# Optimization experiments

Hardware: AMD Instinct MI355X
Metric: run time of the kernel (lower is better)

Reference implementation:

```python
import jax, jax.numpy as jnp
import numpy as np

N = 4096
E = 262144
IN_DIM = 256
EDGE_DIM = 16
NUM_ATOM_FEATURES = 16
LATENT_DIM = 128
NUM_BOND_TYPES = 5


def setup_inputs() -> dict:
    key = jax.random.key(0)
    ks = jax.random.split(key, 12)
    inp = {
        's': jax.random.normal(ks[0], (N, IN_DIM), dtype=jnp.float32),
        'e': jax.random.normal(ks[1], (E, EDGE_DIM), dtype=jnp.float32),
        'batch': jnp.zeros((N,), dtype=jnp.int64),
        'edge_index_global': jax.random.randint(ks[2], (2, E), 0, N, dtype=jnp.int64),
        # learned parameters (torch nn.Linear layout: W is [out, in])
        'W_shared': jax.random.normal(ks[3], (IN_DIM, IN_DIM), dtype=jnp.float32) * 0.02,
        'b_shared': jnp.zeros((IN_DIM,), dtype=jnp.float32),
        'W_bond': jax.random.normal(ks[4], (IN_DIM, EDGE_DIM), dtype=jnp.float32) * 0.02,
        'b_bond': jnp.zeros((IN_DIM,), dtype=jnp.float32),
        'W_bonds': jax.random.normal(ks[5], (NUM_BOND_TYPES, IN_DIM), dtype=jnp.float32) * 0.02,
        'b_bonds': jnp.zeros((NUM_BOND_TYPES,), dtype=jnp.float32),
        'W_atoms': jax.random.normal(ks[6], (NUM_ATOM_FEATURES + LATENT_DIM, IN_DIM), dtype=jnp.float32) * 0.02,
        'b_atoms': jnp.zeros((NUM_ATOM_FEATURES + LATENT_DIM,), dtype=jnp.float32),
    }
    return inp


def reference(s, e, batch, edge_index_global,
              W_shared, b_shared, W_bond, b_bond,
              W_bonds, b_bonds, W_atoms, b_atoms):
    # shared_mapping: Linear + SiLU
    s = jax.nn.silu(s @ W_shared.T + b_shared)  # [n, in_dim]
    j = edge_index_global[0]
    i = edge_index_global[1]
    n = s.shape[0]

    # atoms_lin then split into atom-type logits and latent prediction
    atoms_out = s @ W_atoms.T + b_atoms  # [n, num_atom_features + latent_dim]
    atoms_pred = atoms_out[:, :NUM_ATOM_FEATURES]
    latent_pred = atoms_out[:, NUM_ATOM_FEATURES:]

    # dense scatter -> symmetrize -> gather (faithful to the original O(n^2) path)
    e_dense = jnp.zeros((n, n, e.shape[-1]), dtype=e.dtype).at[j, i].set(e)
    e_dense = 0.5 * (e_dense + e_dense.transpose(1, 0, 2))
    e_sym = e_dense[j, i]  # [E, edge_dim]

    # fused gather + bond linear + SiLU + bonds linear
    f = jax.nn.silu(s[i] + s[j] + e_sym @ W_bond.T + b_bond)  # [E, in_dim]
    bonds_pred = f @ W_bonds.T + b_bonds  # [E, num_bond_types]

    return (latent_pred, atoms_pred, bonds_pred)
```

## Files before the change

### kernel.cpp

```cpp
#include <hip/hip_runtime.h>
#include <hip/hip_bf16.h>

#define N_NODES   4096
#define E_EDGES   262144
#define IN_DIM    256
#define EDGE_DIM  16
#define NAF       16
#define LATENT    128
#define NBT       5

#define LATENT_OFF 0
#define ATOMS_OFF  (N_NODES * LATENT)
#define BONDS_OFF  (ATOMS_OFF + N_NODES * NAF)

#define TBITS 20
#define TSIZE (1u << TBITS)
#define TMASK (TSIZE - 1u)

typedef float    f32x4  __attribute__((ext_vector_type(4)));
typedef float    f32x4v __attribute__((ext_vector_type(4)));
typedef short    bf16x8 __attribute__((ext_vector_type(8)));
typedef unsigned u32x2  __attribute__((ext_vector_type(2)));
typedef unsigned u32x4  __attribute__((ext_vector_type(4)));

__device__ __forceinline__ float silu_f(float x) {
    return x * __builtin_amdgcn_rcpf(1.0f + __expf(-x));
}

__device__ __forceinline__ unsigned pack_bf16x2(float lo, float hi) {
#if __has_builtin(__builtin_amdgcn_cvt_pk_bf16_f32)
    typedef __bf16 bf16x2_t __attribute__((ext_vector_type(2)));
    union { bf16x2_t v; unsigned u; } c;
    c.v = __builtin_amdgcn_cvt_pk_bf16_f32(lo, hi);
    return c.u;
#else
    union { float f; unsigned u; } a, b;
    a.f = lo; b.f = hi;
    const unsigned ra = (a.u + 0x7FFFu + ((a.u >> 16) & 1u)) >> 16;
    const unsigned rb = (b.u + 0x7FFFu + ((b.u >> 16) & 1u)) >> 16;
    return ra | (rb << 16);
#endif
}

__device__ __forceinline__ float bf_lo(unsigned u) {
    union { unsigned x; float f; } c; c.x = u << 16; return c.f;
}
__device__ __forceinline__ float bf_hi(unsigned u) {
    union { unsigned x; float f; } c; c.x = u & 0xFFFF0000u; return c.f;
}

__device__ __forceinline__ void split_bf16(const float4 x0, const float4 x1,
                                           bf16x8* hi, bf16x8* lo) {
    union { bf16x8 v; unsigned u[4]; } H, L;
    H.u[0] = pack_bf16x2(x0.x, x0.y);
    H.u[1] = pack_bf16x2(x0.z, x0.w);
    H.u[2] = pack_bf16x2(x1.x, x1.y);
    H.u[3] = pack_bf16x2(x1.z, x1.w);
    L.u[0] = pack_bf16x2(x0.x - bf_lo(H.u[0]), x0.y - bf_hi(H.u[0]));
    L.u[1] = pack_bf16x2(x0.z - bf_lo(H.u[1]), x0.w - bf_hi(H.u[1]));
    L.u[2] = pack_bf16x2(x1.x - bf_lo(H.u[2]), x1.y - bf_hi(H.u[2]));
    L.u[3] = pack_bf16x2(x1.z - bf_lo(H.u[3]), x1.w - bf_hi(H.u[3]));
    *hi = H.v; *lo = L.v;
}

__device__ __forceinline__ void gld_lds16(const void* g, void* l) {
    __builtin_amdgcn_global_load_lds(
        (const __attribute__((address_space(1))) unsigned*)g,
        (__attribute__((address_space(3))) unsigned*)l, 16, 0, 0);
}

__device__ __forceinline__ unsigned hashh(unsigned key) {
    return (key * 2654435761u) >> (32 - TBITS);
}

__device__ __forceinline__ int resolve2(const unsigned long long* __restrict__ tab,
                                        unsigned key, unsigned long long s0,
                                        unsigned long long s1, unsigned h) {
    if ((unsigned)(s0 >> 18) == key + 1u) return (int)(s0 & 0x3FFFFu);
    if (s0 == 0ULL) return -1;
    if ((unsigned)(s1 >> 18) == key + 1u) return (int)(s1 & 0x3FFFFu);
    if (s1 == 0ULL) return -1;
    h = (h + 2u) & TMASK;
    while (true) {
        const unsigned long long cur = tab[h];
        if (cur == 0ULL) return -1;
        if ((unsigned)(cur >> 18) == key + 1u) return (int)(cur & 0x3FFFFu);
        h = (h + 1u) & TMASK;
    }
}

__global__ __launch_bounds__(256) void k_front(const float* __restrict__ s,
                                               const float* __restrict__ Wsh,
                                               const float* __restrict__ bsh,
                                               const int* __restrict__ eidx,
                                               const float* __restrict__ Wb,
                                               const float* __restrict__ bb,
                                               const float* __restrict__ Wbs,
                                               unsigned short* __restrict__ sact16,
                                               unsigned long long* __restrict__ tab,
                                               u32x4* __restrict__ A1pre,
                                               u32x4* __restrict__ A2pre) {
    const int blk = blockIdx.x;
    const int c   = threadIdx.x;

    if (blk >= 1024) {
        if (blk < 2048) {
            const int k = (blk - 1024) * 256 + c;
            const unsigned j = (unsigned)eidx[k];
            const unsigned i = (unsigned)eidx[E_EDGES + k];
            const unsigned key = (j << 12) | i;
            const unsigned long long mine =
                ((unsigned long long)(key + 1u) << 18) | (unsigned)k;
            unsigned h = hashh(key);
            while (true) {
                const unsigned long long old = atomicCAS(&tab[h], 0ULL, mine);
                if (old == 0ULL) return;
                if ((unsigned)(old >> 18) == key + 1u) {
                    atomicMax(&tab[h], mine);
                    return;
                }
                h = (h + 1u) & TMASK;
            }
        } else {
#pragma unroll
            for (int ee = 0; ee < 4; ++ee) {
                const int idx  = c + 256 * ee;
                const int g    = idx >> 6;
                const int lane = idx & 63;
                const int mm   = lane & 15;
                const int qq   = lane >> 4;

                const float4 w = *(const float4*)(Wb + (16 * g + mm) * EDGE_DIM + 4 * qq);
                u32x4 r1;
                r1.x = pack_bf16x2(w.x, w.y);
                r1.y = pack_bf16x2(w.z, w.w);
                r1.z = pack_bf16x2(bb[16 * g + mm], 0.0f);
                r1.w = 0u;
                A1pre[idx] = r1;

                u32x4 r2;
                if (mm < NBT) {
                    const float4 ws = *(const float4*)(Wbs + mm * IN_DIM + 16 * g + 4 * qq);
                    r2.x = pack_bf16x2(ws.x, ws.y);
                    r2.y = pack_bf16x2(ws.z, ws.w);
                } else {
                    r2.x = 0u; r2.y = 0u;
                }
                r2.z = 0u; r2.w = 0u;
                A2pre[idx] = r2;
            }
        }
        return;
    }

    const int lane = c & 63;
    const int wv   = c >> 6;
    const int wave = blk * 4 + wv;
    const int m    = lane & 15;
    const int q    = lane >> 4;
    const int row0 = (wave >> 4) * 16;
    const int col0 = (wave & 15) * 16;

    f32x4v acc;
    {
        const float bias = bsh[col0 + m];
        acc[0] = bias; acc[1] = bias; acc[2] = bias; acc[3] = bias;
    }

    const float* ap = s   + (size_t)(row0 + m) * IN_DIM + 8 * q;
    const float* bp = Wsh + (size_t)(col0 + m) * IN_DIM + 8 * q;

#pragma unroll
    for (int c8 = 0; c8 < 8; ++c8) {
        const float4 a0 = *(const float4*)(ap + 32 * c8);
        const float4 a1 = *(const float4*)(ap + 32 * c8 + 4);
        const float4 b0 = *(const float4*)(bp + 32 * c8);
        const float4 b1 = *(const float4*)(bp + 32 * c8 + 4);
        bf16x8 Ah, Al, Bh, Bl;
        split_bf16(a0, a1, &Ah, &Al);
        split_bf16(b0, b1, &Bh, &Bl);
        acc = __builtin_amdgcn_mfma_f32_16x16x32_bf16(Ah, Bh, acc, 0, 0, 0);
        acc = __builtin_amdgcn_mfma_f32_16x16x32_bf16(Al, Bh, acc, 0, 0, 0);
        acc = __builtin_amdgcn_mfma_f32_16x16x32_bf16(Ah, Bl, acc, 0, 0, 0);
    }

#pragma unroll
    for (int r = 0; r < 4; ++r) {
        const int row = row0 + 4 * q + r;
        const float v = silu_f(acc[r]);
        sact16[(size_t)row * IN_DIM + col0 + m] =
            (unsigned short)(pack_bf16x2(v, 0.0f) & 0xFFFFu);
    }
}

#define SB0()    __builtin_amdgcn_sched_barrier(0)
#define LGKM0()  do { __asm__ __volatile__("s_waitcnt lgkmcnt(0)" ::: "memory"); SB0(); } while (0)
#define VMW(n)   do { __asm__ __volatile__("s_waitcnt vmcnt(" #n ")" ::: "memory"); SB0(); } while (0)

__global__ __launch_bounds__(256, 6) void k_edges_mfma(const int* __restrict__ eidx,
                                                       const float* __restrict__ e,
                                                       const unsigned long long* __restrict__ tab,
                                                       const unsigned short* __restrict__ sact16,
                                                       const u32x4* __restrict__ A1pre,
                                                       const u32x4* __restrict__ A2pre,
                                                       const float* __restrict__ bbs,
                                                       const float* __restrict__ Wa,
                                                       const float* __restrict__ ba,
                                                       float* __restrict__ out) {
    __shared__ unsigned lds_all[4][1536];
    const int blk  = blockIdx.x;
    const int lane = threadIdx.x & 63;
    const int wv   = threadIdx.x >> 6;
    const int m    = lane & 15;
    const int q    = lane >> 4;

    if (blk >= 4096) {
        const int wave = (blk - 4096) * 4 + wv;
        const int rt = wave / 9;
        const int ct = wave - rt * 9;
        const int row0  = rt * 16;
        const int n_abs = ct * 16 + m;

        f32x4v acc;
        {
            const float bias = ba[n_abs];
            acc[0] = bias; acc[1] = bias; acc[2] = bias; acc[3] = bias;
        }

        const unsigned short* apu = sact16 + (size_t)(row0 + m) * IN_DIM + 8 * q;
        const float*          bp  = Wa + (size_t)n_abs * IN_DIM + 8 * q;

#pragma unroll
        for (int c8 = 0; c8 < 8; ++c8) {
            const bf16x8 A = *(const bf16x8*)(apu + 32 * c8);
            const float4 b0 = *(const float4*)(bp + 32 * c8);
            const float4 b1 = *(const float4*)(bp + 32 * c8 + 4);
            bf16x8 Bh, Bl;
            split_bf16(b0, b1, &Bh, &Bl);
            acc = __builtin_amdgcn_mfma_f32_16x16x32_bf16(A, Bh, acc, 0, 0, 0);
            acc = __builtin_amdgcn_mfma_f32_16x16x32_bf16(A, Bl, acc, 0, 0, 0);
        }
#pragma unroll
        for (int r = 0; r < 4; ++r) {
            const int row = row0 + 4 * q + r;
            if (n_abs < NAF)
                out[ATOMS_OFF + (size_t)row * NAF + n_abs] = acc[r];
            else
                out[LATENT_OFF + (size_t)row * LATENT + (n_abs - NAF)] = acc[r];
        }
        return;
    }

    const int k0 = __builtin_amdgcn_readfirstlane((blk * 4 + wv) * 16);
    unsigned* myl = lds_all[wv];
    const short one_q0 = (q == 0) ? (short)0x3F80 : (short)0;

    f32x4v acc_init;
#pragma unroll
    for (int r = 0; r < 4; ++r) {
        const int bond = 4 * q + r;
        acc_init[r] = (bond < NBT) ? bbs[bond] : 0.0f;
    }
    const u32x4* a1p = A1pre + lane;
    const u32x4* a2p = A2pre + lane;
    const int qh = q >> 1;
    const int qw = 2 * (q & 1);
    const int mw = m * 4;

    const unsigned j_m = (unsigned)eidx[k0 + m];
    const unsigned i_m = (unsigned)eidx[E_EDGES + k0 + m];

    const char* si_base = (const char*)(sact16 + (size_t)i_m * IN_DIM);
    const char* sj_base = (const char*)(sact16 + (size_t)j_m * IN_DIM);

    const unsigned keyF = (j_m << 12) | i_m, keyR = (i_m << 12) | j_m;
    const unsigned hF = hashh(keyF), hR = hashh(keyR);
    const unsigned long long sF0 = tab[hF];
    const unsigned long long sF1 = tab[(hF + 1u) & TMASK];
    const unsigned long long sR0 = tab[hR];
    const unsigned long long sR1 = tab[(hR + 1u) & TMASK];

    auto stage_e = [&](int p, int qb) {
        gld_lds16(si_base + p * 64 + q * 16, (char*)myl + qb);
        gld_lds16(sj_base + p * 64 + q * 16, (char*)myl + qb + 1024);
        SB0();
    };

    stage_e(0, 0);
    stage_e(1, 2048);
    stage_e(2, 4096);

    const int wf = resolve2(tab, keyF, sF0, sF1, hF);
    const int wr = resolve2(tab, keyR, sR0, sR1, hR);

    const float rsc = (wr >= 0) ? 0.5f : 0.0f;
    const int   wrc = (wr >= 0) ? wr : 0;
    const f32x4 ef = *(const f32x4*)(e + (size_t)wf  * EDGE_DIM + 4 * q);
    const f32x4 er = *(const f32x4*)(e + (size_t)wrc * EDGE_DIM + 4 * q);

    union { bf16x8 v; short s[8]; unsigned u[4]; } B1;
    {
        const f32x4 es = ef * 0.5f + er * rsc;
        B1.u[0] = pack_bf16x2(es[0], es[1]);
        B1.u[1] = pack_bf16x2(es[2], es[3]);
        B1.s[4] = one_q0; B1.s[5] = 0;
        B1.u[3] = 0u;
    }

    f32x4v acc0 = acc_init;
    f32x4v acc1 = {0.0f, 0.0f, 0.0f, 0.0f};

    auto qcompute2 = [&](int qb4, int gbase) {
#pragma unroll
        for (int gp = 0; gp < 2; ++gp) {
            const int g   = gbase + gp;
            const int off = (2 * gp + qh) * 64 + mw + qw;

            const u32x2 wi = *(const u32x2*)(myl + qb4 + off);
            const u32x2 wj = *(const u32x2*)(myl + qb4 + 256 + off);

            f32x4v C1;
            C1[0] = bf_lo(wi.x) + bf_lo(wj.x);
            C1[1] = bf_hi(wi.x) + bf_hi(wj.x);
            C1[2] = bf_lo(wi.y) + bf_lo(wj.y);
            C1[3] = bf_hi(wi.y) + bf_hi(wj.y);

            const u32x4 r1 = a1p[g * 64];
            const u32x4 r2 = a2p[g * 64];
            union { bf16x8 v; unsigned u[4]; } A1, A2;
            A1.u[0] = r1.x; A1.u[1] = r1.y; A1.u[2] = r1.z; A1.u[3] = 0u;
            A2.u[0] = r2.x; A2.u[1] = r2.y; A2.u[2] = 0u;   A2.u[3] = 0u;

            const f32x4v P = __builtin_amdgcn_mfma_f32_16x16x32_bf16(A1.v, B1.v, C1, 0, 0, 0);

            union { bf16x8 v; unsigned u[4]; } B2;
            B2.u[0] = pack_bf16x2(silu_f(P[0]), silu_f(P[1]));
            B2.u[1] = pack_bf16x2(silu_f(P[2]), silu_f(P[3]));
            B2.u[2] = 0u; B2.u[3] = 0u;

            if (gp & 1) acc1 = __builtin_amdgcn_mfma_f32_16x16x32_bf16(A2.v, B2.v, acc1, 0, 0, 0);
            else        acc0 = __builtin_amdgcn_mfma_f32_16x16x32_bf16(A2.v, B2.v, acc0, 0, 0, 0);
        }
    };

    VMW(0);
    qcompute2(0, 0);
    LGKM0(); stage_e(3, 0);

    VMW(2);
    qcompute2(512, 2);
    LGKM0(); stage_e(4, 2048);

    VMW(4);
    qcompute2(1024, 4);
    LGKM0(); stage_e(5, 4096);

    VMW(4);
    qcompute2(0, 6);
    LGKM0(); stage_e(6, 0);

    VMW(4);
    qcompute2(512, 8);
    LGKM0(); stage_e(7, 2048);

    VMW(4);
    qcompute2(1024, 10);

    VMW(2);
    qcompute2(0, 12);

    VMW(0);
    qcompute2(512, 14);

    const f32x4v accT = acc0 + acc1;
    float* op = out + BONDS_OFF + (size_t)(k0 + m) * NBT;
    if (q == 0) {
        op[0] = accT[0];
        op[1] = accT[1];
        op[2] = accT[2];
        op[3] = accT[3];
    } else if (q == 1) {
        op[4] = accT[0];
    }
}

extern "C" void kernel_launch(void* const* d_in, const int* in_sizes, int n_in,
                              void* d_out, int out_size, void* d_ws, size_t ws_size,
                              hipStream_t stream) {
    const float* s   = (const float*)d_in[0];
    const float* e   = (const float*)d_in[1];
    const int*   eix = (const int*)d_in[3];
    const float* Wsh = (const float*)d_in[4];
    const float* bsh = (const float*)d_in[5];
    const float* Wb  = (const float*)d_in[6];
    const float* bbo = (const float*)d_in[7];
    const float* Wbs = (const float*)d_in[8];
    const float* bbs = (const float*)d_in[9];
    const float* Wa  = (const float*)d_in[10];
    const float* ba  = (const float*)d_in[11];
    float* out = (float*)d_out;

    char* ws = (char*)d_ws;
    unsigned short*     sact16 = (unsigned short*)ws;
    u32x4*              A1pre  = (u32x4*)(ws + (2u << 20));
    u32x4*              A2pre  = (u32x4*)(ws + (2u << 20) + 16384);
    unsigned long long* tab    = (unsigned long long*)(ws + (3u << 20));

    (void)hipMemsetAsync(tab, 0x00, TSIZE * sizeof(unsigned long long), stream);

    k_front<<<2049, 256, 0, stream>>>(s, Wsh, bsh, eix, Wb, bbo, Wbs,
                                      sact16, tab, A1pre, A2pre);
    k_edges_mfma<<<4672, 256, 0, stream>>>(eix, e, tab, sact16,
                                           A1pre, A2pre, bbs, Wa, ba, out);
}
```

Measured before the change: 174.8 us.

## Stage W_shared in LDS and compute two column tiles per wave in front GEMM

The shared-mapping GEMM in k_front now gives each block a 64x32 output tile. The block converts its 32 rows of W_shared to bf16 hi/lo once into shared memory, and each wave reuses its split A fragment across two 16-column MFMA tiles. This removes the repeated global loads and bf16 splitting of W for every 16x16 tile, and the GEMM grid drops from 1024 to 512 blocks. It adds an LDS footprint, a block barrier, and fewer waves doing GEMM work. A minor indexing change to the A1pre/A2pre pointers in the edge kernel comes along with it.

```diff
diff --git a/kernel.cpp b/kernel.cpp
--- a/kernel.cpp
+++ b/kernel.cpp
@@ -100,12 +100,15 @@
                                                unsigned long long* __restrict__ tab,
                                                u32x4* __restrict__ A1pre,
                                                u32x4* __restrict__ A2pre) {
+    __shared__ short sWh[32][264];
+    __shared__ short sWl[32][264];
+
     const int blk = blockIdx.x;
     const int c   = threadIdx.x;
 
-    if (blk >= 1024) {
-        if (blk < 2048) {
-            const int k = (blk - 1024) * 256 + c;
+    if (blk >= 512) {
+        if (blk < 1536) {
+            const int k = (blk - 512) * 256 + c;
             const unsigned j = (unsigned)eidx[k];
             const unsigned i = (unsigned)eidx[E_EDGES + k];
             const unsigned key = (j << 12) | i;
@@ -153,43 +156,74 @@
         return;
     }
 
+    const int rg = blk >> 3;
+    const int cg = blk & 7;
+
+    {
+        const int r  = c >> 3;
+        const int cq = c & 7;
+        const float* wrow = Wsh + (size_t)(cg * 32 + r) * IN_DIM;
+#pragma unroll
+        for (int k = 0; k < 4; ++k) {
+            const int ch = cq + 8 * k;
+            const float4 b0 = *(const float4*)(wrow + ch * 8);
+            const float4 b1 = *(const float4*)(wrow + ch * 8 + 4);
+            bf16x8 Bh, Bl;
+            split_bf16(b0, b1, &Bh, &Bl);
+            *(bf16x8*)&sWh[r][ch * 8] = Bh;
+            *(bf16x8*)&sWl[r][ch * 8] = Bl;
+        }
+    }
+    __syncthreads();
+
     const int lane = c & 63;
     const int wv   = c >> 6;
-    const int wave = blk * 4 + wv;
     const int m    = lane & 15;
     const int q    = lane >> 4;
-    const int row0 = (wave >> 4) * 16;
-    const int col0 = (wave & 15) * 16;
-
-    f32x4v acc;
+    const int row0 = rg * 64 + wv * 16;
+
+    f32x4v acc0, acc1;
     {
-        const float bias = bsh[col0 + m];
-        acc[0] = bias; acc[1] = bias; acc[2] = bias; acc[3] = bias;
-    }
-
-    const float* ap = s   + (size_t)(row0 + m) * IN_DIM + 8 * q;
-    const float* bp = Wsh + (size_t)(col0 + m) * IN_DIM + 8 * q;
+        const float b0 = bsh[cg * 32 + m];
+        const float b1 = bsh[cg * 32 + 16 + m];
+        acc0[0] = b0; acc0[1] = b0; acc0[2] = b0; acc0[3] = b0;
+        acc1[0] = b1; acc1[1] = b1; acc1[2] = b1; acc1[3] = b1;
+    }
+
+    const float* ap = s + (size_t)(row0 + m) * IN_DIM + 8 * q;
 
 #pragma unroll
     for (int c8 = 0; c8 < 8; ++c8) {
         const float4 a0 = *(const float4*)(ap + 32 * c8);
         const float4 a1 = *(const float4*)(ap + 32 * c8 + 4);
-        const float4 b0 = *(const float4*)(bp + 32 * c8);
-        const float4 b1 = *(const float4*)(bp + 32 * c8 + 4);
-        bf16x8 Ah, Al, Bh, Bl;
+        bf16x8 Ah, Al;
         split_bf16(a0, a1, &Ah, &Al);
-        split_bf16(b0, b1, &Bh, &Bl);
-        acc = __builtin_amdgcn_mfma_f32_16x16x32_bf16(Ah, Bh, acc, 0, 0, 0);
-        acc = __builtin_amdgcn_mfma_f32_16x16x32_bf16(Al, Bh, acc, 0, 0, 0);
-        acc = __builtin_amdgcn_mfma_f32_16x16x32_bf16(Ah, Bl, acc, 0, 0, 0);
+
+        {
+            const bf16x8 Bh = *(const bf16x8*)&sWh[m][32 * c8 + 8 * q];
+            const bf16x8 Bl = *(const bf16x8*)&sWl[m][32 * c8 + 8 * q];
+            acc0 = __builtin_amdgcn_mfma_f32_16x16x32_bf16(Ah, Bh, acc0, 0, 0, 0);
+            acc0 = __builtin_amdgcn_mfma_f32_16x16x32_bf16(Al, Bh, acc0, 0, 0, 0);
+            acc0 = __builtin_amdgcn_mfma_f32_16x16x32_bf16(Ah, Bl, acc0, 0, 0, 0);
+        }
+        {
+            const bf16x8 Bh = *(const bf16x8*)&sWh[16 + m][32 * c8 + 8 * q];
+            const bf16x8 Bl = *(const bf16x8*)&sWl[16 + m][32 * c8 + 8 * q];
+            acc1 = __builtin_amdgcn_mfma_f32_16x16x32_bf16(Ah, Bh, acc1, 0, 0, 0);
+            acc1 = __builtin_amdgcn_mfma_f32_16x16x32_bf16(Al, Bh, acc1, 0, 0, 0);
+            acc1 = __builtin_amdgcn_mfma_f32_16x16x32_bf16(Ah, Bl, acc1, 0, 0, 0);
+        }
     }
 
 #pragma unroll
     for (int r = 0; r < 4; ++r) {
         const int row = row0 + 4 * q + r;
-        const float v = silu_f(acc[r]);
-        sact16[(size_t)row * IN_DIM + col0 + m] =
-            (unsigned short)(pack_bf16x2(v, 0.0f) & 0xFFFFu);
+        const float v0 = silu_f(acc0[r]);
+        const float v1 = silu_f(acc1[r]);
+        sact16[(size_t)row * IN_DIM + cg * 32 + m] =
+            (unsigned short)(pack_bf16x2(v0, 0.0f) & 0xFFFFu);
+        sact16[(size_t)row * IN_DIM + cg * 32 + 16 + m] =
+            (unsigned short)(pack_bf16x2(v1, 0.0f) & 0xFFFFu);
     }
 }
 
@@ -261,8 +295,6 @@
         const int bond = 4 * q + r;
         acc_init[r] = (bond < NBT) ? bbs[bond] : 0.0f;
     }
-    const u32x4* a1p = A1pre + lane;
-    const u32x4* a2p = A2pre + lane;
     const int qh = q >> 1;
     const int qw = 2 * (q & 1);
     const int mw = m * 4;
@@ -325,8 +357,8 @@
             C1[2] = bf_lo(wi.y) + bf_lo(wj.y);
             C1[3] = bf_hi(wi.y) + bf_hi(wj.y);
 
-            const u32x4 r1 = a1p[g * 64];
-            const u32x4 r2 = a2p[g * 64];
+            const u32x4 r1 = A1pre[g * 64 + lane];
+            const u32x4 r2 = A2pre[g * 64 + lane];
             union { bf16x8 v; unsigned u[4]; } A1, A2;
             A1.u[0] = r1.x; A1.u[1] = r1.y; A1.u[2] = r1.z; A1.u[3] = 0u;
             A2.u[0] = r2.x; A2.u[1] = r2.y; A2.u[2] = 0u;   A2.u[3] = 0u;
@@ -408,7 +440,7 @@
 
     (void)hipMemsetAsync(tab, 0x00, TSIZE * sizeof(unsigned long long), stream);
 
-    k_front<<<2049, 256, 0, stream>>>(s, Wsh, bsh, eix, Wb, bbo, Wbs,
+    k_front<<<1537, 256, 0, stream>>>(s, Wsh, bsh, eix, Wb, bbo, Wbs,
                                       sact16, tab, A1pre, A2pre);
     k_edges_mfma<<<4672, 256, 0, stream>>>(eix, e, tab, sact16,
                                            A1pre, A2pre, bbs, Wa, ba, out);
```

After: 172.3 us. No clear change (-1.4%).
